# Performance work log

Measured on AMD Instinct MI355X. Metric: run time of the kernel, lower is better.

## Reference

```python
import jax, jax.numpy as jnp
import numpy as np

N_NODES = 50000   # gates in the circuit batch
N_HOPS = 100000   # number of k-hop cones
MAX_PI = 8        # max PIs per hop (padded, masked via stats == -1)
D = 128           # token_emb / hidden
D_FF = 4 * D      # cls_head hidden width (512)
TT = 64           # max_tt_len -> logits width
LN_EPS = 1e-5


def setup_inputs() -> dict:
    key = jax.random.key(0)
    ks = jax.random.split(key, 8)
    hf = jax.random.normal(ks[0], (N_NODES, D), jnp.float32)
    all_hop_pi = jax.random.randint(ks[1], (N_HOPS, MAX_PI), 0, N_NODES)
    # stats in {-1, 0, 1}; -1 marks an invalid (padded) PI slot
    all_hop_pi_stats = jax.random.randint(ks[2], (N_HOPS, MAX_PI), 0, 3) - 1
    all_hop_po = jax.random.randint(ks[3], (N_HOPS,), 0, N_NODES)
    w_q = jax.random.normal(ks[4], (D,), jnp.float32) / np.sqrt(D)
    W1 = jax.random.normal(ks[5], (D, D_FF), jnp.float32) / np.sqrt(D)
    b1 = jnp.zeros((D_FF,), jnp.float32)
    gamma = jnp.ones((D_FF,), jnp.float32)
    beta = jnp.zeros((D_FF,), jnp.float32)
    W2 = jax.random.normal(ks[6], (D_FF, TT), jnp.float32) / np.sqrt(D_FF)
    b2 = jnp.zeros((TT,), jnp.float32)
    return {
        'hf': hf, 'w_q': w_q, 'W1': W1, 'b1': b1, 'gamma': gamma,
        'beta': beta, 'W2': W2, 'b2': b2,
        'all_hop_pi': all_hop_pi, 'all_hop_pi_stats': all_hop_pi_stats,
        'all_hop_po': all_hop_po,
    }


def reference(hf, w_q, W1, b1, gamma, beta, W2, b2,
              all_hop_pi, all_hop_pi_stats, all_hop_po):
    # Per-hop gather: valid PI embeddings + PO embedding -> [H, P+1, D]
    pi_tok = hf[all_hop_pi]                       # [H, P, D]
    po_tok = hf[all_hop_po][:, None, :]           # [H, 1, D]
    tokens = jnp.concatenate([pi_tok, po_tok], axis=1)
    valid = jnp.concatenate(
        [all_hop_pi_stats != -1,
         jnp.ones((all_hop_po.shape[0], 1), bool)], axis=1)  # [H, P+1]
    # tf_Pooling: masked single-query attention pooling over the ragged set
    scores = jnp.einsum('hpd,d->hp', tokens, w_q) / jnp.sqrt(jnp.float32(D))
    scores = jnp.where(valid, scores, jnp.float32(-1e30))
    attn = jax.nn.softmax(scores, axis=-1)
    hop_hf = jnp.einsum('hp,hpd->hd', attn, tokens)  # [H, D]
    # cls_head: Linear(D, 4D) -> ReLU -> LayerNorm(4D) -> Linear(4D, TT)
    h = jax.nn.relu(hop_hf @ W1 + b1)
    mu = jnp.mean(h, axis=-1, keepdims=True)
    var = jnp.var(h, axis=-1, keepdims=True)
    h = (h - mu) * jax.lax.rsqrt(var + LN_EPS) * gamma + beta
    logits = h @ W2 + b2                           # [H, TT]
    return logits
```

## Files before the change

kernel.cpp:

```cpp
#include <hip/hip_runtime.h>
#include <hip/hip_bf16.h>
#include <math.h>

#define DIM 128
#define DFF 512
#define TTW 64
#define NPI 8
#define NTOK 9
#define TILE_H 32

typedef __attribute__((ext_vector_type(8))) short short8;
typedef __attribute__((ext_vector_type(4))) float float4v;

__device__ __forceinline__ float bf16lo_f32(unsigned u) {
    union { unsigned u; float f; } v; v.u = u << 16;
    return v.f;
}
__device__ __forceinline__ float bf16hi_f32(unsigned u) {
    union { unsigned u; float f; } v; v.u = u & 0xffff0000u;
    return v.f;
}
__device__ __forceinline__ unsigned pk_bf16(float a, float b) {
    __hip_bfloat162 h = __float22bfloat162_rn(float2{a, b});
    union { __hip_bfloat162 h; unsigned u; } cv; cv.h = h;
    return cv.u;
}

__global__ __launch_bounds__(256)
void prep_k(const float* __restrict__ hf, const float* __restrict__ W1,
            const float* __restrict__ W2, const float* __restrict__ gamma,
            const float* __restrict__ beta, const float* __restrict__ b2,
            unsigned short* __restrict__ hf2, unsigned short* __restrict__ w1t,
            unsigned short* __restrict__ w2g,
            float* __restrict__ C1, float* __restrict__ C2,
            int n_hf, int B_HF)
{
    __shared__ float tile[32][33];
    const int b = blockIdx.x, t = threadIdx.x;
    if (b < B_HF) {
        int i = (b * 256 + t) * 8;
        if (i < n_hf) {
            float4v v0 = *(const float4v*)(hf + i);
            float4v v1 = *(const float4v*)(hf + i + 4);
            uint4 o;
            o.x = pk_bf16(v0[0], v0[1]);
            o.y = pk_bf16(v0[2], v0[3]);
            o.z = pk_bf16(v1[0], v1[1]);
            o.w = pk_bf16(v1[2], v1[3]);
            *(uint4*)(hf2 + i) = o;
        }
    } else if (b < B_HF + 64) {
        const int tb = b - B_HF;
        const int r0 = (tb & 3) * 32, c0 = (tb >> 2) * 32;
        const int ty = t >> 3, tx = t & 7;
        *(float4v*)&tile[ty][tx * 4] = *(const float4v*)(W1 + (r0 + ty) * DFF + c0 + tx * 4);
        __syncthreads();
        uint2 o;
        o.x = pk_bf16(tile[tx * 4 + 0][ty], tile[tx * 4 + 1][ty]);
        o.y = pk_bf16(tile[tx * 4 + 2][ty], tile[tx * 4 + 3][ty]);
        *(uint2*)(w1t + (c0 + ty) * DIM + r0 + tx * 4) = o;
    } else if (b < B_HF + 96) {
        const int tb = b - B_HF - 64;
        const int r0 = (tb & 15) * 32, c0 = (tb >> 4) * 32;
        const int ty = t >> 3, tx = t & 7;
        const float g = gamma[r0 + ty];
        float4v v = *(const float4v*)(W2 + (r0 + ty) * TTW + c0 + tx * 4);
        v[0] *= g; v[1] *= g; v[2] *= g; v[3] *= g;
        *(float4v*)&tile[ty][tx * 4] = v;
        __syncthreads();
        uint2 o;
        o.x = pk_bf16(tile[tx * 4 + 0][ty], tile[tx * 4 + 1][ty]);
        o.y = pk_bf16(tile[tx * 4 + 2][ty], tile[tx * 4 + 3][ty]);
        *(uint2*)(w2g + (c0 + ty) * DFF + r0 + tx * 4) = o;
    } else {
        if (t < TTW) {
            float c1 = 0.f, c2 = 0.f;
            for (int k = 0; k < DFF; ++k) {
                float w = W2[k * TTW + t];
                c1 += gamma[k] * w;
                c2 += beta[k] * w;
            }
            C1[t] = c1;
            C2[t] = b2[t] + c2;
        }
    }
}

__global__ __launch_bounds__(256)
void fused_k(const unsigned short* __restrict__ hf2,
             const float* __restrict__ w_q,
             const int* __restrict__ pi,
             const int* __restrict__ stats,
             const int* __restrict__ po,
             const unsigned short* __restrict__ w1t,
             const float* __restrict__ b1,
             const unsigned short* __restrict__ w2g,
             const float* __restrict__ C1,
             const float* __restrict__ C2,
             float* __restrict__ out,
             int H)
{
    __shared__ __align__(16) unsigned short Apool[TILE_H][DIM + 8];
    __shared__ __align__(16) unsigned short Hsm[TILE_H][256 + 8];
    __shared__ float part[2][16][4][2];
    __shared__ float2 mursm[TILE_H];

    const int t    = threadIdx.x;
    const int lane = t & 63;
    const int w    = t >> 6;
    const int row  = lane & 15;
    const int quad = lane >> 4;
    const int hop0 = blockIdx.x * TILE_H;

    {
        const int g = t >> 5, l = t & 31;
        const float4v wq4 = *(const float4v*)(w_q + l * 4);

        int idxs[4][NTOK];
        unsigned vm[4];
        #pragma unroll
        for (int it = 0; it < 4; ++it) {
            int hop = hop0 + g + it * 8;
            if (hop >= H) hop = H - 1;
            int4 p0 = *(const int4*)(pi + hop * NPI);
            int4 p1 = *(const int4*)(pi + hop * NPI + 4);
            int4 s0 = *(const int4*)(stats + hop * NPI);
            int4 s1 = *(const int4*)(stats + hop * NPI + 4);
            idxs[it][0] = p0.x; idxs[it][1] = p0.y;
            idxs[it][2] = p0.z; idxs[it][3] = p0.w;
            idxs[it][4] = p1.x; idxs[it][5] = p1.y;
            idxs[it][6] = p1.z; idxs[it][7] = p1.w;
            idxs[it][8] = po[hop];
            vm[it] = (s0.x != -1 ? 1u   : 0u) | (s0.y != -1 ? 2u   : 0u)
                   | (s0.z != -1 ? 4u   : 0u) | (s0.w != -1 ? 8u   : 0u)
                   | (s1.x != -1 ? 16u  : 0u) | (s1.y != -1 ? 32u  : 0u)
                   | (s1.z != -1 ? 64u  : 0u) | (s1.w != -1 ? 128u : 0u)
                   | 256u;
        }
        uint2 tu[4][NTOK];
        #pragma unroll
        for (int it = 0; it < 4; ++it)
            #pragma unroll
            for (int p = 0; p < NTOK; ++p)
                tu[it][p] = *(const uint2*)(hf2 + (size_t)idxs[it][p] * DIM + l * 4);

        #pragma unroll
        for (int it = 0; it < 4; ++it) {
            const int hl = g + it * 8;
            float tok[NTOK][4];
            #pragma unroll
            for (int p = 0; p < NTOK; ++p) {
                tok[p][0] = bf16lo_f32(tu[it][p].x);
                tok[p][1] = bf16hi_f32(tu[it][p].x);
                tok[p][2] = bf16lo_f32(tu[it][p].y);
                tok[p][3] = bf16hi_f32(tu[it][p].y);
            }
            float sc[NTOK];
            #pragma unroll
            for (int p = 0; p < NTOK; ++p)
                sc[p] = tok[p][0]*wq4[0] + tok[p][1]*wq4[1]
                      + tok[p][2]*wq4[2] + tok[p][3]*wq4[3];
            #pragma unroll
            for (int m = 1; m < 32; m <<= 1) {
                #pragma unroll
                for (int p = 0; p < NTOK; ++p) sc[p] += __shfl_xor(sc[p], m);
            }
            const float isd = 0.08838834764831845f;
            float mx = -1e30f;
            #pragma unroll
            for (int p = 0; p < NTOK; ++p) {
                sc[p] = ((vm[it] >> p) & 1u) ? sc[p] * isd : -1e30f;
                mx = fmaxf(mx, sc[p]);
            }
            float se = 0.f;
            #pragma unroll
            for (int p = 0; p < NTOK; ++p) { sc[p] = __expf(sc[p] - mx); se += sc[p]; }
            const float inv = 1.f / se;
            float a0=0.f, a1=0.f, a2=0.f, a3=0.f;
            #pragma unroll
            for (int p = 0; p < NTOK; ++p) {
                float a = sc[p] * inv;
                a0 += a * tok[p][0]; a1 += a * tok[p][1];
                a2 += a * tok[p][2]; a3 += a * tok[p][3];
            }
            uint2 o;
            o.x = pk_bf16(a0, a1);
            o.y = pk_bf16(a2, a3);
            *(uint2*)&Apool[hl][l * 4] = o;
        }
    }
    __syncthreads();

    float4v acc[8][2];
    #pragma unroll
    for (int mt = 0; mt < 8; ++mt) {
        acc[mt][0] = (float4v){0.f, 0.f, 0.f, 0.f};
        acc[mt][1] = (float4v){0.f, 0.f, 0.f, 0.f};
    }
    {
        short8 bfr[2][4];
        #pragma unroll
        for (int ks = 0; ks < 4; ++ks) {
            const int k0 = ks * 32 + quad * 8;
            #pragma unroll
            for (int ht = 0; ht < 2; ++ht)
                bfr[ht][ks] = *(const short8*)&Apool[ht * 16 + row][k0];
        }
        #pragma unroll
        for (int mt = 0; mt < 8; ++mt) {
            const unsigned short* wrow = w1t + (size_t)(mt * 64 + w * 16 + row) * DIM;
            #pragma unroll
            for (int ks = 0; ks < 4; ++ks) {
                short8 afr = *(const short8*)(wrow + ks * 32 + quad * 8);
                acc[mt][0] = __builtin_amdgcn_mfma_f32_16x16x32_bf16(afr, bfr[0][ks], acc[mt][0], 0, 0, 0);
                acc[mt][1] = __builtin_amdgcn_mfma_f32_16x16x32_bf16(afr, bfr[1][ks], acc[mt][1], 0, 0, 0);
            }
        }
    }
    float sum0 = 0.f, ssq0 = 0.f, sum1 = 0.f, ssq1 = 0.f;
    uint2 pk[8][2];
    #pragma unroll
    for (int mt = 0; mt < 8; ++mt) {
        const int nb = mt * 64 + w * 16 + quad * 4;
        const float4v bias = *(const float4v*)(b1 + nb);
        float o0[4], o1[4];
        #pragma unroll
        for (int r = 0; r < 4; ++r) {
            o0[r] = fmaxf(acc[mt][0][r] + bias[r], 0.f);
            o1[r] = fmaxf(acc[mt][1][r] + bias[r], 0.f);
            sum0 += o0[r];  ssq0 += o0[r] * o0[r];
            sum1 += o1[r];  ssq1 += o1[r] * o1[r];
        }
        pk[mt][0].x = pk_bf16(o0[0], o0[1]);  pk[mt][0].y = pk_bf16(o0[2], o0[3]);
        pk[mt][1].x = pk_bf16(o1[0], o1[1]);  pk[mt][1].y = pk_bf16(o1[2], o1[3]);
    }
    #pragma unroll
    for (int m = 16; m <= 32; m <<= 1) {
        sum0 += __shfl_xor(sum0, m);  ssq0 += __shfl_xor(ssq0, m);
        sum1 += __shfl_xor(sum1, m);  ssq1 += __shfl_xor(ssq1, m);
    }
    if (lane < 16) {
        part[0][row][w][0] = sum0;  part[0][row][w][1] = ssq0;
        part[1][row][w][0] = sum1;  part[1][row][w][1] = ssq1;
    }
    __syncthreads();
    {
        const float invn = 1.f / (float)DFF;
        float mu0, rs0, mu1, rs1;
        {
            float S = 0.f, Q = 0.f;
            #pragma unroll
            for (int ww = 0; ww < 4; ++ww) { S += part[0][row][ww][0]; Q += part[0][row][ww][1]; }
            mu0 = S * invn;  rs0 = rsqrtf(Q * invn - mu0 * mu0 + 1e-5f);
        }
        {
            float S = 0.f, Q = 0.f;
            #pragma unroll
            for (int ww = 0; ww < 4; ++ww) { S += part[1][row][ww][0]; Q += part[1][row][ww][1]; }
            mu1 = S * invn;  rs1 = rsqrtf(Q * invn - mu1 * mu1 + 1e-5f);
        }
        if (t < 16) {
            mursm[t]      = float2{mu0, rs0};
            mursm[16 + t] = float2{mu1, rs1};
        }
    }
    {
        float4v acc2[2];
        acc2[0] = (float4v){0.f,0.f,0.f,0.f};
        acc2[1] = (float4v){0.f,0.f,0.f,0.f};
        #pragma unroll
        for (int c = 0; c < 2; ++c) {
            #pragma unroll
            for (int m4 = 0; m4 < 4; ++m4) {
                const int col = m4 * 64 + w * 16 + quad * 4;
                *(uint2*)&Hsm[0 * 16 + row][col] = pk[c * 4 + m4][0];
                *(uint2*)&Hsm[1 * 16 + row][col] = pk[c * 4 + m4][1];
            }
            __syncthreads();
            const unsigned short* w2row = w2g + (size_t)(w * 16 + row) * DFF + c * 256;
            #pragma unroll
            for (int ks = 0; ks < 8; ++ks) {
                const int k0 = ks * 32 + quad * 8;
                short8 bfr = *(const short8*)(w2row + k0);
                #pragma unroll
                for (int mt = 0; mt < 2; ++mt) {
                    short8 afr = *(const short8*)&Hsm[mt * 16 + row][k0];
                    acc2[mt] = __builtin_amdgcn_mfma_f32_16x16x32_bf16(
                        afr, bfr, acc2[mt], 0, 0, 0);
                }
            }
            if (c == 0) __syncthreads();
        }
        const int tt = w * 16 + row;
        const float c1v = C1[tt];
        const float c2v = C2[tt];
        #pragma unroll
        for (int mt = 0; mt < 2; ++mt) {
            #pragma unroll
            for (int r = 0; r < 4; ++r) {
                const int hl = mt * 16 + quad * 4 + r;
                int hop = hop0 + hl;
                if (hop < H) {
                    float2 mr = mursm[hl];
                    out[(size_t)hop * TTW + tt] = mr.y * (acc2[mt][r] - mr.x * c1v) + c2v;
                }
            }
        }
    }
}

extern "C" void kernel_launch(void* const* d_in, const int* in_sizes, int n_in,
                              void* d_out, int out_size, void* d_ws, size_t ws_size,
                              hipStream_t stream) {
    const float* hf    = (const float*)d_in[0];
    const float* w_q   = (const float*)d_in[1];
    const float* W1    = (const float*)d_in[2];
    const float* b1    = (const float*)d_in[3];
    const float* gamma = (const float*)d_in[4];
    const float* beta  = (const float*)d_in[5];
    const float* W2    = (const float*)d_in[6];
    const float* b2    = (const float*)d_in[7];
    const int* pi      = (const int*)d_in[8];
    const int* stats   = (const int*)d_in[9];
    const int* po      = (const int*)d_in[10];
    float* out         = (float*)d_out;

    const int n_hf = in_sizes[0];
    const int H    = in_sizes[10];
    const int ntiles = (H + TILE_H - 1) / TILE_H;

    char* ws = (char*)d_ws;
    unsigned short* w1t = (unsigned short*)ws;
    unsigned short* w2g = (unsigned short*)(ws + 131072);
    unsigned short* hf2 = (unsigned short*)(ws + 196608);
    float* C1 = (float*)(ws + 196608 + (size_t)n_hf * 2);
    float* C2 = C1 + TTW;

    const int B_HF = (n_hf + 2047) / 2048;
    hipLaunchKernelGGL(prep_k, dim3(B_HF + 97), dim3(256), 0, stream,
                       hf, W1, W2, gamma, beta, b2, hf2, w1t, w2g, C1, C2, n_hf, B_HF);
    hipLaunchKernelGGL(fused_k, dim3(ntiles), dim3(256), 0, stream,
                       hf2, w_q, pi, stats, po, w1t, b1, w2g, C1, C2, out, H);
}
```

Baseline: 238.6 us.

## Split fused pooling+MLP kernel into separate gather-pool and MLP kernels

Moves the attention-pooling gather out of the fused kernel into its own kernel. That kernel uses one 32-lane group per hop and writes the pooled bf16 vectors to the output buffer, which serves as scratch. A second kernel loads these pooled tiles into LDS and runs the MLP. The aim is higher occupancy and better latency hiding for the random gathers, which no longer share registers and LDS with the MFMA stage. The cost is an extra global write and read of the pooled activations plus one more kernel launch, and the second kernel writes its logits into the same buffer it reads from.

```diff
diff --git a/kernel.cpp b/kernel.cpp
--- a/kernel.cpp
+++ b/kernel.cpp
@@ -87,18 +87,88 @@
 }
 
 __global__ __launch_bounds__(256)
-void fused_k(const unsigned short* __restrict__ hf2,
-             const float* __restrict__ w_q,
-             const int* __restrict__ pi,
-             const int* __restrict__ stats,
-             const int* __restrict__ po,
-             const unsigned short* __restrict__ w1t,
-             const float* __restrict__ b1,
-             const unsigned short* __restrict__ w2g,
-             const float* __restrict__ C1,
-             const float* __restrict__ C2,
-             float* __restrict__ out,
-             int H)
+void pool_k(const unsigned short* __restrict__ hf2,
+            const float* __restrict__ w_q,
+            const int* __restrict__ pi,
+            const int* __restrict__ stats,
+            const int* __restrict__ po,
+            uint2* apool,
+            int H)
+{
+    const int t = threadIdx.x;
+    const int g = t >> 5, l = t & 31;
+    const int hop = blockIdx.x * 8 + g;
+    if (hop >= H) return;
+
+    const float4v wq4 = *(const float4v*)(w_q + l * 4);
+    const int4 p0 = *(const int4*)(pi + hop * NPI);
+    const int4 p1 = *(const int4*)(pi + hop * NPI + 4);
+    const int4 s0 = *(const int4*)(stats + hop * NPI);
+    const int4 s1 = *(const int4*)(stats + hop * NPI + 4);
+    const int ipo = po[hop];
+
+    uint2 tu[NTOK];
+    tu[0] = *(const uint2*)(hf2 + (size_t)p0.x * DIM + l * 4);
+    tu[1] = *(const uint2*)(hf2 + (size_t)p0.y * DIM + l * 4);
+    tu[2] = *(const uint2*)(hf2 + (size_t)p0.z * DIM + l * 4);
+    tu[3] = *(const uint2*)(hf2 + (size_t)p0.w * DIM + l * 4);
+    tu[4] = *(const uint2*)(hf2 + (size_t)p1.x * DIM + l * 4);
+    tu[5] = *(const uint2*)(hf2 + (size_t)p1.y * DIM + l * 4);
+    tu[6] = *(const uint2*)(hf2 + (size_t)p1.z * DIM + l * 4);
+    tu[7] = *(const uint2*)(hf2 + (size_t)p1.w * DIM + l * 4);
+    tu[8] = *(const uint2*)(hf2 + (size_t)ipo * DIM + l * 4);
+
+    const unsigned vm = (s0.x != -1 ? 1u   : 0u) | (s0.y != -1 ? 2u   : 0u)
+                      | (s0.z != -1 ? 4u   : 0u) | (s0.w != -1 ? 8u   : 0u)
+                      | (s1.x != -1 ? 16u  : 0u) | (s1.y != -1 ? 32u  : 0u)
+                      | (s1.z != -1 ? 64u  : 0u) | (s1.w != -1 ? 128u : 0u)
+                      | 256u;
+
+    float sc[NTOK];
+    #pragma unroll
+    for (int p = 0; p < NTOK; ++p) {
+        float x0 = bf16lo_f32(tu[p].x), x1 = bf16hi_f32(tu[p].x);
+        float x2 = bf16lo_f32(tu[p].y), x3 = bf16hi_f32(tu[p].y);
+        sc[p] = x0 * wq4[0] + x1 * wq4[1] + x2 * wq4[2] + x3 * wq4[3];
+    }
+    #pragma unroll
+    for (int m = 1; m < 32; m <<= 1) {
+        #pragma unroll
+        for (int p = 0; p < NTOK; ++p) sc[p] += __shfl_xor(sc[p], m);
+    }
+    const float isd = 0.08838834764831845f;
+    float mx = -1e30f;
+    #pragma unroll
+    for (int p = 0; p < NTOK; ++p) {
+        sc[p] = ((vm >> p) & 1u) ? sc[p] * isd : -1e30f;
+        mx = fmaxf(mx, sc[p]);
+    }
+    float se = 0.f;
+    #pragma unroll
+    for (int p = 0; p < NTOK; ++p) { sc[p] = __expf(sc[p] - mx); se += sc[p]; }
+    const float inv = 1.f / se;
+    float a0 = 0.f, a1 = 0.f, a2 = 0.f, a3 = 0.f;
+    #pragma unroll
+    for (int p = 0; p < NTOK; ++p) {
+        const float a = sc[p] * inv;
+        a0 += a * bf16lo_f32(tu[p].x);  a1 += a * bf16hi_f32(tu[p].x);
+        a2 += a * bf16lo_f32(tu[p].y);  a3 += a * bf16hi_f32(tu[p].y);
+    }
+    uint2 o;
+    o.x = pk_bf16(a0, a1);
+    o.y = pk_bf16(a2, a3);
+    apool[(size_t)hop * 32 + l] = o;
+}
+
+__global__ __launch_bounds__(256)
+void mlp_k(const uint4* apool4,
+           const unsigned short* __restrict__ w1t,
+           const float* __restrict__ b1,
+           const unsigned short* __restrict__ w2g,
+           const float* __restrict__ C1,
+           const float* __restrict__ C2,
+           float* out,
+           int H)
 {
     __shared__ __align__(16) unsigned short Apool[TILE_H][DIM + 8];
     __shared__ __align__(16) unsigned short Hsm[TILE_H][256 + 8];
@@ -112,82 +182,12 @@
     const int quad = lane >> 4;
     const int hop0 = blockIdx.x * TILE_H;
 
-    {
-        const int g = t >> 5, l = t & 31;
-        const float4v wq4 = *(const float4v*)(w_q + l * 4);
-
-        int idxs[4][NTOK];
-        unsigned vm[4];
-        #pragma unroll
-        for (int it = 0; it < 4; ++it) {
-            int hop = hop0 + g + it * 8;
-            if (hop >= H) hop = H - 1;
-            int4 p0 = *(const int4*)(pi + hop * NPI);
-            int4 p1 = *(const int4*)(pi + hop * NPI + 4);
-            int4 s0 = *(const int4*)(stats + hop * NPI);
-            int4 s1 = *(const int4*)(stats + hop * NPI + 4);
-            idxs[it][0] = p0.x; idxs[it][1] = p0.y;
-            idxs[it][2] = p0.z; idxs[it][3] = p0.w;
-            idxs[it][4] = p1.x; idxs[it][5] = p1.y;
-            idxs[it][6] = p1.z; idxs[it][7] = p1.w;
-            idxs[it][8] = po[hop];
-            vm[it] = (s0.x != -1 ? 1u   : 0u) | (s0.y != -1 ? 2u   : 0u)
-                   | (s0.z != -1 ? 4u   : 0u) | (s0.w != -1 ? 8u   : 0u)
-                   | (s1.x != -1 ? 16u  : 0u) | (s1.y != -1 ? 32u  : 0u)
-                   | (s1.z != -1 ? 64u  : 0u) | (s1.w != -1 ? 128u : 0u)
-                   | 256u;
-        }
-        uint2 tu[4][NTOK];
-        #pragma unroll
-        for (int it = 0; it < 4; ++it)
-            #pragma unroll
-            for (int p = 0; p < NTOK; ++p)
-                tu[it][p] = *(const uint2*)(hf2 + (size_t)idxs[it][p] * DIM + l * 4);
-
-        #pragma unroll
-        for (int it = 0; it < 4; ++it) {
-            const int hl = g + it * 8;
-            float tok[NTOK][4];
-            #pragma unroll
-            for (int p = 0; p < NTOK; ++p) {
-                tok[p][0] = bf16lo_f32(tu[it][p].x);
-                tok[p][1] = bf16hi_f32(tu[it][p].x);
-                tok[p][2] = bf16lo_f32(tu[it][p].y);
-                tok[p][3] = bf16hi_f32(tu[it][p].y);
-            }
-            float sc[NTOK];
-            #pragma unroll
-            for (int p = 0; p < NTOK; ++p)
-                sc[p] = tok[p][0]*wq4[0] + tok[p][1]*wq4[1]
-                      + tok[p][2]*wq4[2] + tok[p][3]*wq4[3];
-            #pragma unroll
-            for (int m = 1; m < 32; m <<= 1) {
-                #pragma unroll
-                for (int p = 0; p < NTOK; ++p) sc[p] += __shfl_xor(sc[p], m);
-            }
-            const float isd = 0.08838834764831845f;
-            float mx = -1e30f;
-            #pragma unroll
-            for (int p = 0; p < NTOK; ++p) {
-                sc[p] = ((vm[it] >> p) & 1u) ? sc[p] * isd : -1e30f;
-                mx = fmaxf(mx, sc[p]);
-            }
-            float se = 0.f;
-            #pragma unroll
-            for (int p = 0; p < NTOK; ++p) { sc[p] = __expf(sc[p] - mx); se += sc[p]; }
-            const float inv = 1.f / se;
-            float a0=0.f, a1=0.f, a2=0.f, a3=0.f;
-            #pragma unroll
-            for (int p = 0; p < NTOK; ++p) {
-                float a = sc[p] * inv;
-                a0 += a * tok[p][0]; a1 += a * tok[p][1];
-                a2 += a * tok[p][2]; a3 += a * tok[p][3];
-            }
-            uint2 o;
-            o.x = pk_bf16(a0, a1);
-            o.y = pk_bf16(a2, a3);
-            *(uint2*)&Apool[hl][l * 4] = o;
-        }
+    #pragma unroll
+    for (int j = t; j < 512; j += 256) {
+        int gr = hop0 + (j >> 4);
+        if (gr >= H) gr = H - 1;
+        uint4 v = apool4[(size_t)gr * 16 + (j & 15)];
+        *(uint4*)&Apool[j >> 4][(j & 15) * 8] = v;
     }
     __syncthreads();
 
@@ -339,6 +339,8 @@
     const int B_HF = (n_hf + 2047) / 2048;
     hipLaunchKernelGGL(prep_k, dim3(B_HF + 97), dim3(256), 0, stream,
                        hf, W1, W2, gamma, beta, b2, hf2, w1t, w2g, C1, C2, n_hf, B_HF);
-    hipLaunchKernelGGL(fused_k, dim3(ntiles), dim3(256), 0, stream,
-                       hf2, w_q, pi, stats, po, w1t, b1, w2g, C1, C2, out, H);
-}
+    hipLaunchKernelGGL(pool_k, dim3((H + 7) / 8), dim3(256), 0, stream,
+                       hf2, w_q, pi, stats, po, (uint2*)d_out, H);
+    hipLaunchKernelGGL(mlp_k, dim3(ntiles), dim3(256), 0, stream,
+                       (const uint4*)d_out, w1t, b1, w2g, C1, C2, out, H);
+}
```

Result: no change. 235.0 us (-1.5%).
